# Kernel optimization log

Measured on AMD Instinct MI355X. Metric: run time of the kernel, lower is better.

Reference implementation:

```python
import jax, jax.numpy as jnp
import numpy as np

NUM_HEADS, HEAD_DIM = 4, 64
BLOCK_SIZE, S = 32, 4
LENGTHS = np.array([2048, 1024, 1536, 512, 2048, 1280, 1792, 768])
MAX_LEN = int(LENGTHS.max())            # 2048
NUM_BLOCKS = MAX_LEN // BLOCK_SIZE      # 64
B = len(LENGTHS)
T = int(LENGTHS.sum())                  # 11008
HIDDEN = NUM_HEADS * HEAD_DIM           # 256
SCALE = HEAD_DIM ** -0.5
INV_SCALE = 1.0 / SCALE
EPS = 1e-6


def setup_inputs() -> dict:
    key = jax.random.key(0)
    ks = jax.random.split(key, 6)
    offsets = np.concatenate([[0], np.cumsum(LENGTHS)]).astype(np.int64)
    batch_ids = np.repeat(np.arange(B), LENGTHS).astype(np.int64)
    pos_ids = np.concatenate([np.arange(l) for l in LENGTHS]).astype(np.int64)
    shp = (T, NUM_HEADS, HEAD_DIM)
    return {
        "q": jax.random.normal(ks[0], shp, jnp.float32),
        "k": jax.random.normal(ks[1], shp, jnp.float32),
        "v": jax.random.normal(ks[2], shp, jnp.float32),
        "u": jax.random.normal(ks[3], shp, jnp.float32),
        "Wg_cmp": jax.random.normal(ks[4], (NUM_HEADS, HEAD_DIM), jnp.float32) * 0.1,
        "Wg_slc": jax.random.normal(ks[5], (NUM_HEADS, HEAD_DIM), jnp.float32) * 0.1,
        "x_offsets": jnp.asarray(offsets),
        "batch_ids": jnp.asarray(batch_ids),
        "pos_ids": jnp.asarray(pos_ids),
    }


def _silu(x):
    return x * jax.nn.sigmoid(x)


def _layer_norm(x):
    # non-affine LayerNorm over last dim, eps=1e-6
    mu = jnp.mean(x, -1, keepdims=True)
    var = jnp.mean(jnp.square(x - mu), -1, keepdims=True)
    return (x - mu) / jnp.sqrt(var + EPS)


def _forward(q, k, v, u, Wg_cmp, Wg_slc, x_offsets, batch_ids, pos_ids):
    # jagged -> padded dense [B, MAX_LEN, H, D]
    pad = lambda x: jnp.zeros((B, MAX_LEN, NUM_HEADS, HEAD_DIM), x.dtype).at[batch_ids, pos_ids].set(x)
    pq, pk, pv = pad(q), pad(k), pad(v)

    # gate model: per-head sigmoid linear gates from padded_q; g_slc is unused
    # by the original forward (the slc kernel never consumes it)
    g_cmp = jax.nn.sigmoid(jnp.einsum('bnhd,hd->bnh', pq, Wg_cmp))
    _g_slc = jax.nn.sigmoid(jnp.einsum('bnhd,hd->bnh', pq, Wg_slc))
    g_cmp_jag = g_cmp[batch_ids, pos_ids]  # [T, H]

    # block-compressed K/V: mean over zero-padded blocks of size BLOCK_SIZE
    k_cmp = pk.reshape(B, NUM_BLOCKS, BLOCK_SIZE, NUM_HEADS, HEAD_DIM).mean(2)
    v_cmp = pv.reshape(B, NUM_BLOCKS, BLOCK_SIZE, NUM_HEADS, HEAD_DIM).mean(2)

    # SiLU-activated block-causal compressed attention
    raw = jnp.einsum('bnhd,bmhd->bnhm', pq, k_cmp) * SCALE  # [B, n, H, m]
    q_blk = jnp.arange(MAX_LEN) // BLOCK_SIZE
    k_blk = jnp.arange(NUM_BLOCKS)
    causal = q_blk[:, None] >= k_blk[None, :]   # [MAX_LEN, NUM_BLOCKS]
    local = q_blk[:, None] == k_blk[None, :]
    p_cmp = jnp.where(causal[None, :, None, :], _silu(raw) * INV_SCALE, 0.0)

    # top-S block selection; local block score forced to 1.0; odd slots
    # duplicated from even slots (as in source)
    sel = jnp.where(local[None, :, None, :], 1.0, p_cmp)
    topk = jax.lax.top_k(sel, S)[1]             # [B, MAX_LEN, H, S]
    topk = topk.at[..., 1::2].set(topk[..., 0::2])
    topk_jag = topk[batch_ids, pos_ids]         # [T, H, S]

    # compressed-branch output, gathered to jagged and gated by g_cmp
    o_cmp = jnp.einsum('bnhm,bmhd->bnhd', p_cmp, v_cmp)[batch_ids, pos_ids]
    o_cmp = o_cmp * g_cmp_jag[:, :, None]       # [T, H, D]

    # selected branch: per-row, per-head gather of S blocks of raw K/V
    seq_start = x_offsets[batch_ids]            # [T]
    head_ix = jnp.arange(NUM_HEADS)[None, :, None]
    o_slc = jnp.zeros_like(q)
    for s in range(S):  # fixed small S, duplicates intentionally double-count
        b_idx = topk_jag[:, :, s]               # [T, H]
        pos_in_seq = b_idx[:, :, None] * BLOCK_SIZE + jnp.arange(BLOCK_SIZE)  # [T,H,BS]
        valid = (b_idx[:, :, None] >= 0) & (pos_in_seq <= pos_ids[:, None, None])
        tgt = jnp.clip(seq_start[:, None, None] + pos_in_seq, 0, T - 1)
        k_g = k[tgt, head_ix]                   # [T, H, BS, D]
        score = jnp.einsum('thd,thbd->thb', q, k_g) * SCALE
        p = jnp.where(valid, _silu(score) * INV_SCALE, 0.0)
        v_g = v[tgt, head_ix]                   # [T, H, BS, D]
        o_slc = o_slc + jnp.einsum('thb,thbd->thd', p, v_g)

    # per-token LayerNorm over hidden, scaled by u, then branch sum
    o_cmp = _layer_norm(o_cmp.reshape(T, HIDDEN)).reshape(T, NUM_HEADS, HEAD_DIM) * u
    o_slc = _layer_norm(o_slc.reshape(T, HIDDEN)).reshape(T, NUM_HEADS, HEAD_DIM) * u
    return (o_cmp + o_slc).reshape(T, HIDDEN)


def reference(q, k, v, u, Wg_cmp, Wg_slc, x_offsets, batch_ids, pos_ids):
    return _forward(q, k, v, u, Wg_cmp, Wg_slc, x_offsets, batch_ids, pos_ids)
```

## Files before the change

### kernel.cpp

```cpp
#include <hip/hip_runtime.h>
#include <math.h>

#define NH 4
#define HD 64
#define HIDDEN 256
#define BS 32
#define NB 64
#define SCALE 0.125f
#define INV_SCALE 8.0f

__device__ __forceinline__ float fast_sigmoid(float x) {
    return 1.0f / (1.0f + __expf(-x));
}
__device__ __forceinline__ float readlane_f(float v, int lane) {
    return __int_as_float(__builtin_amdgcn_readlane(__float_as_int(v), lane));
}

__global__ __launch_bounds__(256) void kcmp_kernel(
    const float* __restrict__ k, const float* __restrict__ v,
    const int* __restrict__ x_offsets,
    double* __restrict__ k_cmp, float* __restrict__ v_cmp2) {
    int bb  = blockIdx.x;
    int b   = bb >> 6;
    int blk = bb & 63;
    int tid = threadIdx.x;
    int s0   = x_offsets[b];
    int len  = x_offsets[b + 1] - s0;
    int nblk = len >> 5;
    int h = tid >> 6, d = tid & 63;
    if (blockIdx.y == 0) {
        double acc = 0.0;
        if (blk < nblk) {
            const float* kp = k + (size_t)(s0 + blk * BS) * HIDDEN + tid;
            #pragma unroll
            for (int i = 0; i < BS; ++i) acc += (double)kp[i * HIDDEN];
            acc *= (1.0 / BS);
        }
        k_cmp[((size_t)(b * NH + h) * 64 + blk) * 64 + d] = acc;
    } else {
        float acc = 0.f;
        if (blk < nblk) {
            const float* vp = v + (size_t)(s0 + blk * BS) * HIDDEN + tid;
            #pragma unroll
            for (int i = 0; i < BS; ++i) acc += vp[i * HIDDEN];
            acc *= (1.0f / BS);
        }
        v_cmp2[((size_t)(b * NH + h) * 32 + (blk >> 1)) * 128 + d * 2 + (blk & 1)] = acc;
    }
}

__global__ __launch_bounds__(256, 3) void cmp_kernel(
    const float* __restrict__ q,
    const int* __restrict__ batch_ids, const int* __restrict__ pos_ids,
    const double* __restrict__ k_cmp, const float* __restrict__ v_cmp2,
    float* __restrict__ oc_buf, int2* __restrict__ idxbuf, int T) {
    int t0   = blockIdx.x * 64;
    int h    = blockIdx.y;
    int tid  = threadIdx.x;
    int wv   = __builtin_amdgcn_readfirstlane(tid >> 6);
    int lane = tid & 63;
    int b    = batch_ids[t0];
    int pos0 = pos_ids[t0];

    __shared__ __align__(16) char smem[49920];
    float* qs = (float*)smem;
    float* ps = qs + 64 * 65;
    float* vs = ps + 64 * 66;
    unsigned long long* trip = (unsigned long long*)qs;

    const float* qg = q + (size_t)t0 * HIDDEN + h * HD;
    #pragma unroll
    for (int i = 0; i < 16; ++i) {
        int idx = tid + 256 * i;
        int tok = idx >> 6, dd = idx & 63;
        qs[dd * 65 + tok] = qg[(size_t)tok * HIDDEN + dd];
    }
    const float* vg = v_cmp2 + (size_t)(b * NH + h) * 4096;
    #pragma unroll
    for (int i = 0; i < 16; ++i) vs[tid + 256 * i] = vg[tid + 256 * i];
    __syncthreads();

    int qblk_max = (pos0 + 63) >> 5;
    int m_need   = qblk_max + 2;
    if (m_need > 63) m_need = 63;

    unsigned long long a0 = 0ull, a1 = 0ull, a2 = 0ull;
    if (16 * wv <= m_need) {
        double qd[64];
        #pragma unroll
        for (int dd = 0; dd < 64; ++dd) qd[dd] = (double)qs[dd * 65 + lane];
        int myqblk = (pos0 + lane) >> 5;

        const double* kcb = k_cmp + ((size_t)(b * NH + h) * 64 + wv * 16) * 64;
        #pragma unroll
        for (int mi = 0; mi < 16; ++mi) {
            int m = wv * 16 + mi;
            const double* kr = kcb + mi * 64;
            double accA = 0.0, accB = 0.0;
            #pragma unroll
            for (int dd = 0; dd < 32; ++dd) {
                accA += qd[2 * dd]     * kr[2 * dd];
                accB += qd[2 * dd + 1] * kr[2 * dd + 1];
            }
            double r = (accA + accB) * 0.125;
            double p64 = 0.0;
            if (m <= myqblk) p64 = r / (1.0 + exp(-r)) * 8.0;
            double selv = (m == myqblk) ? 1.0 : p64;
            ps[lane * 66 + m] = (float)p64;
            long long sb = __double_as_longlong(selv);
            unsigned long long kk = (unsigned long long)sb;
            kk = (sb < 0) ? ~kk : (kk | 0x8000000000000000ull);
            kk = (kk & ~63ull) | (unsigned long long)(63 - m);
            if (kk > a0)      { a2 = a1; a1 = a0; a0 = kk; }
            else if (kk > a1) { a2 = a1; a1 = kk; }
            else if (kk > a2) { a2 = kk; }
        }
    }
    __syncthreads();
    trip[(wv * 64 + lane) * 3 + 0] = a0;
    trip[(wv * 64 + lane) * 3 + 1] = a1;
    trip[(wv * 64 + lane) * 3 + 2] = a2;
    __syncthreads();

    if (wv == 0) {
        unsigned long long kk2[4][3];
        #pragma unroll
        for (int w = 0; w < 4; ++w)
            #pragma unroll
            for (int j = 0; j < 3; ++j)
                kk2[w][j] = trip[(w * 64 + lane) * 3 + j];
        int pp[4] = {0, 0, 0, 0};
        int outi[3];
        #pragma unroll
        for (int s = 0; s < 3; ++s) {
            unsigned long long best = 0ull; int bw = 0;
            #pragma unroll
            for (int w = 0; w < 4; ++w) {
                unsigned long long hd_ = (pp[w] == 0) ? kk2[w][0]
                                       : (pp[w] == 1) ? kk2[w][1] : kk2[w][2];
                if (hd_ > best) { best = hd_; bw = w; }
            }
            outi[s] = 63 - (int)(best & 63ull);
            #pragma unroll
            for (int w = 0; w < 4; ++w) if (w == bw) pp[w]++;
        }
        idxbuf[(size_t)(t0 + lane) * NH + h] = make_int2(outi[0], outi[2]);
    }

    float occ[16];
    #pragma unroll
    for (int tt = 0; tt < 16; ++tt) occ[tt] = 0.f;
    int mmax2 = qblk_max >> 1;
    const float2* vs2 = (const float2*)vs;
    for (int m2 = 0; m2 <= mmax2; ++m2) {
        float2 vv = vs2[m2 * 64 + lane];
        #pragma unroll
        for (int tt = 0; tt < 16; ++tt) {
            int tok = wv * 16 + tt;
            float2 pv = *(const float2*)(ps + tok * 66 + 2 * m2);
            occ[tt] += pv.x * vv.x + pv.y * vv.y;
        }
    }
    #pragma unroll
    for (int tt = 0; tt < 16; ++tt)
        oc_buf[(size_t)(t0 + wv * 16 + tt) * HIDDEN + h * HD + lane] = occ[tt];
}

__global__ __launch_bounds__(64) void build_kernel(
    const int* __restrict__ pos_ids, const int2* __restrict__ idxbuf,
    int* __restrict__ cnt_arr, int2* __restrict__ entries,
    float* __restrict__ os_out, int T) {
    int wg   = blockIdx.x;
    int qb   = wg >> 2;
    int h    = wg & 3;
    int t0   = qb * 32;
    int lane = threadIdx.x;

    int pos0 = pos_ids[t0];
    int qblk = pos0 >> 5;

    float* ob = os_out + (size_t)t0 * HIDDEN + h * HD + lane;
    #pragma unroll
    for (int tk = 0; tk < 32; ++tk) ob[(size_t)tk * HIDDEN] = 0.f;

    int myi0 = -1, myi2 = -1;
    unsigned long long U = 0ull;
    if (lane < 32) {
        int2 ix = idxbuf[(size_t)(t0 + lane) * NH + h];
        myi0 = ix.x;
        myi2 = (ix.y <= qblk) ? ix.y : -1;
        U = (1ull << myi0);
        if (myi2 >= 0) U |= (1ull << myi2);
    }
    #pragma unroll
    for (int off = 1; off < 64; off <<= 1) U |= __shfl_xor(U, off, 64);

    int slot = 0;
    while (U) {
        int m = (int)__builtin_ctzll(U); U &= U - 1;
        unsigned long long wm = __ballot(lane < 32 && (myi0 == m || myi2 == m));
        if (lane == 0) entries[(size_t)wg * 64 + slot] = make_int2(m, (int)wm);
        slot++;
    }
    if (lane == 0) cnt_arr[wg] = slot;
}

__global__ __launch_bounds__(64, 4) void slc2_kernel(
    const float* __restrict__ q, const float* __restrict__ k,
    const float* __restrict__ v,
    const int* __restrict__ x_offsets, const int* __restrict__ batch_ids,
    const int* __restrict__ pos_ids,
    const int* __restrict__ cnt_arr, const int2* __restrict__ entries,
    float* __restrict__ os_out, int T) {
    int i  = blockIdx.x;
    int wgidx = (i & 7) * (gridDim.x >> 3) + (i >> 3);
    int slot = wgidx & 63;
    int wg   = wgidx >> 6;
    if (slot >= cnt_arr[wg]) return;

    int2 e = entries[(size_t)wg * 64 + slot];
    int m = e.x;
    unsigned int want = (unsigned int)e.y;
    int qb = wg >> 2, h = wg & 3;
    int t0 = qb * 32;
    int lane = threadIdx.x;
    int r = lane & 15, cc = lane >> 4;

    int pos0 = pos_ids[t0];
    int s0   = x_offsets[batch_ids[t0]];

    __shared__ float vs_w[32 * 64];

    const float* kb_p = k + (size_t)(s0 + m * BS) * HIDDEN + h * HD;
    float4 kb0[4], kb1[4];
    #pragma unroll
    for (int j = 0; j < 4; ++j) {
        kb0[j] = *(const float4*)(kb_p + (size_t)r * HIDDEN + (cc + 4 * j) * 4);
        kb1[j] = *(const float4*)(kb_p + (size_t)(16 + r) * HIDDEN + (cc + 4 * j) * 4);
    }
    {
        const float* vb_p = v + (size_t)(s0 + m * BS) * HIDDEN + h * HD + lane;
        #pragma unroll
        for (int g = 0; g < 4; ++g) {
            const float* p0_ = vb_p + (size_t)(g * 8) * HIDDEN;
            float x0 = p0_[0 * HIDDEN], x1 = p0_[1 * HIDDEN];
            float x2 = p0_[2 * HIDDEN], x3 = p0_[3 * HIDDEN];
            float x4 = p0_[4 * HIDDEN], x5 = p0_[5 * HIDDEN];
            float x6 = p0_[6 * HIDDEN], x7 = p0_[7 * HIDDEN];
            float* d0 = vs_w + (g * 8) * 64 + lane;
            d0[0 * 64] = x0; d0[1 * 64] = x1; d0[2 * 64] = x2; d0[3 * 64] = x3;
            d0[4 * 64] = x4; d0[5 * 64] = x5; d0[6 * 64] = x6; d0[7 * 64] = x7;
        }
    }
    #pragma unroll
    for (int j = 0; j < 4; ++j) {
        asm volatile("" : "+v"(kb0[j].x), "+v"(kb0[j].y),
                          "+v"(kb0[j].z), "+v"(kb0[j].w));
        asm volatile("" : "+v"(kb1[j].x), "+v"(kb1[j].y),
                          "+v"(kb1[j].z), "+v"(kb1[j].w));
    }
    int row0 = m * BS + r;

    while (want) {
        int tk0 = (int)__builtin_ctz(want); want &= want - 1;
        int tk1 = -1;
        if (want) { tk1 = (int)__builtin_ctz(want); want &= want - 1; }

        const float4* qr0 = (const float4*)(q + (size_t)(t0 + tk0) * HIDDEN + h * HD);
        const float4* qr1 = (tk1 >= 0)
            ? (const float4*)(q + (size_t)(t0 + tk1) * HIDDEN + h * HD) : qr0;
        float4 qa[4], qb[4];
        #pragma unroll
        for (int j = 0; j < 4; ++j) { qa[j] = qr0[cc + 4 * j]; qb[j] = qr1[cc + 4 * j]; }

        float pa0, pa1, pb0 = 0.f, pb1 = 0.f;
        {
            int pos_tk = pos0 + tk0;
            float psA0 = 0.f, psB0 = 0.f, psA1 = 0.f, psB1 = 0.f;
            #pragma unroll
            for (int j = 0; j < 4; ++j) {
                if (j & 1) {
                    psB0 += qa[j].x * kb0[j].x + qa[j].y * kb0[j].y
                          + qa[j].z * kb0[j].z + qa[j].w * kb0[j].w;
                    psB1 += qa[j].x * kb1[j].x + qa[j].y * kb1[j].y
                          + qa[j].z * kb1[j].z + qa[j].w * kb1[j].w;
                } else {
                    psA0 += qa[j].x * kb0[j].x + qa[j].y * kb0[j].y
                          + qa[j].z * kb0[j].z + qa[j].w * kb0[j].w;
                    psA1 += qa[j].x * kb1[j].x + qa[j].y * kb1[j].y
                          + qa[j].z * kb1[j].z + qa[j].w * kb1[j].w;
                }
            }
            float psum0 = psA0 + psB0, psum1 = psA1 + psB1;
            psum0 += __shfl_xor(psum0, 16, 64); psum0 += __shfl_xor(psum0, 32, 64);
            psum1 += __shfl_xor(psum1, 16, 64); psum1 += __shfl_xor(psum1, 32, 64);
            float scv0 = psum0 * SCALE, scv1 = psum1 * SCALE;
            pa0 = (row0 <= pos_tk)      ? scv0 * fast_sigmoid(scv0) * 16.f : 0.f;
            pa1 = (row0 + 16 <= pos_tk) ? scv1 * fast_sigmoid(scv1) * 16.f : 0.f;
        }
        if (tk1 >= 0) {
            int pos_tk = pos0 + tk1;
            float psA0 = 0.f, psB0 = 0.f, psA1 = 0.f, psB1 = 0.f;
            #pragma unroll
            for (int j = 0; j < 4; ++j) {
                if (j & 1) {
                    psB0 += qb[j].x * kb0[j].x + qb[j].y * kb0[j].y
                          + qb[j].z * kb0[j].z + qb[j].w * kb0[j].w;
                    psB1 += qb[j].x * kb1[j].x + qb[j].y * kb1[j].y
                          + qb[j].z * kb1[j].z + qb[j].w * kb1[j].w;
                } else {
                    psA0 += qb[j].x * kb0[j].x + qb[j].y * kb0[j].y
                          + qb[j].z * kb0[j].z + qb[j].w * kb0[j].w;
                    psA1 += qb[j].x * kb1[j].x + qb[j].y * kb1[j].y
                          + qb[j].z * kb1[j].z + qb[j].w * kb1[j].w;
                }
            }
            float psum0 = psA0 + psB0, psum1 = psA1 + psB1;
            psum0 += __shfl_xor(psum0, 16, 64); psum0 += __shfl_xor(psum0, 32, 64);
            psum1 += __shfl_xor(psum1, 16, 64); psum1 += __shfl_xor(psum1, 32, 64);
            float scv0 = psum0 * SCALE, scv1 = psum1 * SCALE;
            pb0 = (row0 <= pos_tk)      ? scv0 * fast_sigmoid(scv0) * 16.f : 0.f;
            pb1 = (row0 + 16 <= pos_tk) ? scv1 * fast_sigmoid(scv1) * 16.f : 0.f;
        }

        float oA0 = 0.f, oA1 = 0.f, oB0 = 0.f, oB1 = 0.f;
        #pragma unroll
        for (int rr = 0; rr < 16; ++rr) {
            float v0 = vs_w[rr * 64 + lane];
            float v1 = vs_w[(16 + rr) * 64 + lane];
            oA0 += readlane_f(pa0, rr) * v0;  oA1 += readlane_f(pa1, rr) * v1;
            oB0 += readlane_f(pb0, rr) * v0;  oB1 += readlane_f(pb1, rr) * v1;
        }
        atomicAdd(&os_out[(size_t)(t0 + tk0) * HIDDEN + h * HD + lane], oA0 + oA1);
        if (tk1 >= 0)
            atomicAdd(&os_out[(size_t)(t0 + tk1) * HIDDEN + h * HD + lane], oB0 + oB1);
    }
}

__global__ __launch_bounds__(256) void ln_kernel(
    const float* __restrict__ q, const float* __restrict__ u,
    const float* __restrict__ Wg_cmp,
    const float* __restrict__ oc_buf, float* __restrict__ io, int T) {
    int tid = threadIdx.x;
    int grp = tid >> 5;
    int sub = tid & 31;
    int t   = blockIdx.x * 8 + grp;
    int D0  = sub * 8;

    const float4* qp = (const float4*)(q + (size_t)t * HIDDEN + D0);
    float4 qa = qp[0], qb = qp[1];
    const float4* wp = (const float4*)(Wg_cmp + D0);
    float4 wa = wp[0], wb = wp[1];
    float gp = qa.x * wa.x + qa.y * wa.y + qa.z * wa.z + qa.w * wa.w
             + qb.x * wb.x + qb.y * wb.y + qb.z * wb.z + qb.w * wb.w;
    gp += __shfl_xor(gp, 1, 64);
    gp += __shfl_xor(gp, 2, 64);
    gp += __shfl_xor(gp, 4, 64);
    float g = fast_sigmoid(gp);

    const float4* ocp = (const float4*)(oc_buf + (size_t)t * HIDDEN + D0);
    float4 oa = ocp[0], ob = ocp[1];
    oa.x *= g; oa.y *= g; oa.z *= g; oa.w *= g;
    ob.x *= g; ob.y *= g; ob.z *= g; ob.w *= g;
    float4* iop = (float4*)(io + (size_t)t * HIDDEN + D0);
    float4 sa = iop[0], sb = iop[1];

    float sc_ = oa.x + oa.y + oa.z + oa.w + ob.x + ob.y + ob.z + ob.w;
    float sc2 = oa.x * oa.x + oa.y * oa.y + oa.z * oa.z + oa.w * oa.w
              + ob.x * ob.x + ob.y * ob.y + ob.z * ob.z + ob.w * ob.w;
    float ss_ = sa.x + sa.y + sa.z + sa.w + sb.x + sb.y + sb.z + sb.w;
    float ss2 = sa.x * sa.x + sa.y * sa.y + sa.z * sa.z + sa.w * sa.w
              + sb.x * sb.x + sb.y * sb.y + sb.z * sb.z + sb.w * sb.w;
    #pragma unroll
    for (int off = 1; off < 32; off <<= 1) {
        sc_ += __shfl_xor(sc_, off, 64);
        sc2 += __shfl_xor(sc2, off, 64);
        ss_ += __shfl_xor(ss_, off, 64);
        ss2 += __shfl_xor(ss2, off, 64);
    }
    float muc  = sc_ * (1.0f / HIDDEN);
    float varc = sc2 * (1.0f / HIDDEN) - muc * muc;
    float mus  = ss_ * (1.0f / HIDDEN);
    float vars = ss2 * (1.0f / HIDDEN) - mus * mus;
    float rc = rsqrtf(varc + 1e-6f), rs = rsqrtf(vars + 1e-6f);

    const float4* up = (const float4*)(u + (size_t)t * HIDDEN + D0);
    float4 ua = up[0], ub = up[1];
    float4 o0, o1;
    o0.x = ((oa.x - muc) * rc + (sa.x - mus) * rs) * ua.x;
    o0.y = ((oa.y - muc) * rc + (sa.y - mus) * rs) * ua.y;
    o0.z = ((oa.z - muc) * rc + (sa.z - mus) * rs) * ua.z;
    o0.w = ((oa.w - muc) * rc + (sa.w - mus) * rs) * ua.w;
    o1.x = ((ob.x - muc) * rc + (sb.x - mus) * rs) * ub.x;
    o1.y = ((ob.y - muc) * rc + (sb.y - mus) * rs) * ub.y;
    o1.z = ((ob.z - muc) * rc + (sb.z - mus) * rs) * ub.z;
    o1.w = ((ob.w - muc) * rc + (sb.w - mus) * rs) * ub.w;
    iop[0] = o0; iop[1] = o1;
}

extern "C" void kernel_launch(void* const* d_in, const int* in_sizes, int n_in,
                              void* d_out, int out_size, void* d_ws, size_t ws_size,
                              hipStream_t stream) {
    const float* q      = (const float*)d_in[0];
    const float* k      = (const float*)d_in[1];
    const float* v      = (const float*)d_in[2];
    const float* u      = (const float*)d_in[3];
    const float* Wg_cmp = (const float*)d_in[4];
    const int* x_offsets = (const int*)d_in[6];
    const int* batch_ids = (const int*)d_in[7];
    const int* pos_ids   = (const int*)d_in[8];

    int T = in_sizes[0] / HIDDEN;
    int B = in_sizes[6] - 1;

    double* k_cmp  = (double*)d_ws;
    float*  v_cmp2 = (float*)(k_cmp + (size_t)B * NH * 4096);
    float*  oc_buf = v_cmp2 + (size_t)B * NH * 4096;
    int2*   idxbuf = (int2*)(oc_buf + (size_t)T * HIDDEN);
    int2*   entries = idxbuf + (size_t)T * NH;
    int*    cnt_arr = (int*)(entries + (size_t)(T / 32) * NH * 64);

    int nwg = (T / 32) * NH;

    kcmp_kernel<<<dim3(B * NB, 2), 256, 0, stream>>>(k, v, x_offsets, k_cmp, v_cmp2);
    cmp_kernel<<<dim3(T / 64, NH), 256, 0, stream>>>(
        q, batch_ids, pos_ids, k_cmp, v_cmp2, oc_buf, idxbuf, T);
    build_kernel<<<dim3(nwg), 64, 0, stream>>>(
        pos_ids, idxbuf, cnt_arr, entries, (float*)d_out, T);
    slc2_kernel<<<dim3(nwg * 64), 64, 0, stream>>>(
        q, k, v, x_offsets, batch_ids, pos_ids, cnt_arr, entries,
        (float*)d_out, T);
    ln_kernel<<<dim3(T / 8), 256, 0, stream>>>(
        q, u, Wg_cmp, oc_buf, (float*)d_out, T);
}
```

Baseline: 208.3 us.

## Compact selection entries and use persistent work-stealing grid for selection kernel

```diff
diff --git a/kernel.cpp b/kernel.cpp
--- a/kernel.cpp
+++ b/kernel.cpp
@@ -19,11 +19,13 @@
 __global__ __launch_bounds__(256) void kcmp_kernel(
     const float* __restrict__ k, const float* __restrict__ v,
     const int* __restrict__ x_offsets,
-    double* __restrict__ k_cmp, float* __restrict__ v_cmp2) {
+    double* __restrict__ k_cmp, float* __restrict__ v_cmp2,
+    int* __restrict__ counters) {
     int bb  = blockIdx.x;
     int b   = bb >> 6;
     int blk = bb & 63;
     int tid = threadIdx.x;
+    if (bb == 0 && blockIdx.y == 0 && tid < 2) counters[tid] = 0;
     int s0   = x_offsets[b];
     int len  = x_offsets[b + 1] - s0;
     int nblk = len >> 5;
@@ -168,7 +170,7 @@
 
 __global__ __launch_bounds__(64) void build_kernel(
     const int* __restrict__ pos_ids, const int2* __restrict__ idxbuf,
-    int* __restrict__ cnt_arr, int2* __restrict__ entries,
+    int* __restrict__ counters, int2* __restrict__ entries,
     float* __restrict__ os_out, int T) {
     int wg   = blockIdx.x;
     int qb   = wg >> 2;
@@ -195,145 +197,154 @@
     #pragma unroll
     for (int off = 1; off < 64; off <<= 1) U |= __shfl_xor(U, off, 64);
 
+    int nsel = __popcll(U);
+    int base = 0;
+    if (lane == 0) base = atomicAdd(&counters[0], nsel);
+    base = __shfl(base, 0, 64);
+
     int slot = 0;
     while (U) {
         int m = (int)__builtin_ctzll(U); U &= U - 1;
         unsigned long long wm = __ballot(lane < 32 && (myi0 == m || myi2 == m));
-        if (lane == 0) entries[(size_t)wg * 64 + slot] = make_int2(m, (int)wm);
+        if (lane == 0)
+            entries[(size_t)base + slot] = make_int2((wg << 6) | m, (int)wm);
         slot++;
     }
-    if (lane == 0) cnt_arr[wg] = slot;
-}
-
-__global__ __launch_bounds__(64, 4) void slc2_kernel(
+}
+
+__global__ __launch_bounds__(64, 4) void slc3_kernel(
     const float* __restrict__ q, const float* __restrict__ k,
     const float* __restrict__ v,
     const int* __restrict__ x_offsets, const int* __restrict__ batch_ids,
     const int* __restrict__ pos_ids,
-    const int* __restrict__ cnt_arr, const int2* __restrict__ entries,
+    int* __restrict__ counters, const int2* __restrict__ entries,
     float* __restrict__ os_out, int T) {
-    int i  = blockIdx.x;
-    int wgidx = (i & 7) * (gridDim.x >> 3) + (i >> 3);
-    int slot = wgidx & 63;
-    int wg   = wgidx >> 6;
-    if (slot >= cnt_arr[wg]) return;
-
-    int2 e = entries[(size_t)wg * 64 + slot];
-    int m = e.x;
-    unsigned int want = (unsigned int)e.y;
-    int qb = wg >> 2, h = wg & 3;
-    int t0 = qb * 32;
     int lane = threadIdx.x;
     int r = lane & 15, cc = lane >> 4;
-
-    int pos0 = pos_ids[t0];
-    int s0   = x_offsets[batch_ids[t0]];
-
     __shared__ float vs_w[32 * 64];
 
-    const float* kb_p = k + (size_t)(s0 + m * BS) * HIDDEN + h * HD;
-    float4 kb0[4], kb1[4];
-    #pragma unroll
-    for (int j = 0; j < 4; ++j) {
-        kb0[j] = *(const float4*)(kb_p + (size_t)r * HIDDEN + (cc + 4 * j) * 4);
-        kb1[j] = *(const float4*)(kb_p + (size_t)(16 + r) * HIDDEN + (cc + 4 * j) * 4);
-    }
-    {
-        const float* vb_p = v + (size_t)(s0 + m * BS) * HIDDEN + h * HD + lane;
-        #pragma unroll
-        for (int g = 0; g < 4; ++g) {
-            const float* p0_ = vb_p + (size_t)(g * 8) * HIDDEN;
-            float x0 = p0_[0 * HIDDEN], x1 = p0_[1 * HIDDEN];
-            float x2 = p0_[2 * HIDDEN], x3 = p0_[3 * HIDDEN];
-            float x4 = p0_[4 * HIDDEN], x5 = p0_[5 * HIDDEN];
-            float x6 = p0_[6 * HIDDEN], x7 = p0_[7 * HIDDEN];
-            float* d0 = vs_w + (g * 8) * 64 + lane;
-            d0[0 * 64] = x0; d0[1 * 64] = x1; d0[2 * 64] = x2; d0[3 * 64] = x3;
-            d0[4 * 64] = x4; d0[5 * 64] = x5; d0[6 * 64] = x6; d0[7 * 64] = x7;
-        }
-    }
-    #pragma unroll
-    for (int j = 0; j < 4; ++j) {
-        asm volatile("" : "+v"(kb0[j].x), "+v"(kb0[j].y),
-                          "+v"(kb0[j].z), "+v"(kb0[j].w));
-        asm volatile("" : "+v"(kb1[j].x), "+v"(kb1[j].y),
-                          "+v"(kb1[j].z), "+v"(kb1[j].w));
-    }
-    int row0 = m * BS + r;
-
-    while (want) {
-        int tk0 = (int)__builtin_ctz(want); want &= want - 1;
-        int tk1 = -1;
-        if (want) { tk1 = (int)__builtin_ctz(want); want &= want - 1; }
-
-        const float4* qr0 = (const float4*)(q + (size_t)(t0 + tk0) * HIDDEN + h * HD);
-        const float4* qr1 = (tk1 >= 0)
-            ? (const float4*)(q + (size_t)(t0 + tk1) * HIDDEN + h * HD) : qr0;
-        float4 qa[4], qb[4];
-        #pragma unroll
-        for (int j = 0; j < 4; ++j) { qa[j] = qr0[cc + 4 * j]; qb[j] = qr1[cc + 4 * j]; }
-
-        float pa0, pa1, pb0 = 0.f, pb1 = 0.f;
+    int total = counters[0];
+
+    for (;;) {
+        int t_ = 0;
+        if (lane == 0) t_ = atomicAdd(&counters[1], 1);
+        t_ = __shfl(t_, 0, 64);
+        if (t_ >= total) break;
+
+        int2 e = entries[t_];
+        int wg = e.x >> 6;
+        int m  = e.x & 63;
+        unsigned int want = (unsigned int)e.y;
+        int qb = wg >> 2, h = wg & 3;
+        int t0 = qb * 32;
+
+        int pos0 = pos_ids[t0];
+        int s0   = x_offsets[batch_ids[t0]];
+
+        const float* kb_p = k + (size_t)(s0 + m * BS) * HIDDEN + h * HD;
+        float4 kb0[4], kb1[4];
+        #pragma unroll
+        for (int j = 0; j < 4; ++j) {
+            kb0[j] = *(const float4*)(kb_p + (size_t)r * HIDDEN + (cc + 4 * j) * 4);
+            kb1[j] = *(const float4*)(kb_p + (size_t)(16 + r) * HIDDEN + (cc + 4 * j) * 4);
+        }
         {
-            int pos_tk = pos0 + tk0;
-            float psA0 = 0.f, psB0 = 0.f, psA1 = 0.f, psB1 = 0.f;
-            #pragma unroll
-            for (int j = 0; j < 4; ++j) {
-                if (j & 1) {
-                    psB0 += qa[j].x * kb0[j].x + qa[j].y * kb0[j].y
-                          + qa[j].z * kb0[j].z + qa[j].w * kb0[j].w;
-                    psB1 += qa[j].x * kb1[j].x + qa[j].y * kb1[j].y
-                          + qa[j].z * kb1[j].z + qa[j].w * kb1[j].w;
-                } else {
-                    psA0 += qa[j].x * kb0[j].x + qa[j].y * kb0[j].y
-                          + qa[j].z * kb0[j].z + qa[j].w * kb0[j].w;
-                    psA1 += qa[j].x * kb1[j].x + qa[j].y * kb1[j].y
-                          + qa[j].z * kb1[j].z + qa[j].w * kb1[j].w;
+            const float* vb_p = v + (size_t)(s0 + m * BS) * HIDDEN + h * HD + lane;
+            #pragma unroll
+            for (int g = 0; g < 4; ++g) {
+                const float* p0_ = vb_p + (size_t)(g * 8) * HIDDEN;
+                float x0 = p0_[0 * HIDDEN], x1 = p0_[1 * HIDDEN];
+                float x2 = p0_[2 * HIDDEN], x3 = p0_[3 * HIDDEN];
+                float x4 = p0_[4 * HIDDEN], x5 = p0_[5 * HIDDEN];
+                float x6 = p0_[6 * HIDDEN], x7 = p0_[7 * HIDDEN];
+                float* d0 = vs_w + (g * 8) * 64 + lane;
+                d0[0 * 64] = x0; d0[1 * 64] = x1; d0[2 * 64] = x2; d0[3 * 64] = x3;
+                d0[4 * 64] = x4; d0[5 * 64] = x5; d0[6 * 64] = x6; d0[7 * 64] = x7;
+            }
+        }
+        #pragma unroll
+        for (int j = 0; j < 4; ++j) {
+            asm volatile("" : "+v"(kb0[j].x), "+v"(kb0[j].y),
+                              "+v"(kb0[j].z), "+v"(kb0[j].w));
+            asm volatile("" : "+v"(kb1[j].x), "+v"(kb1[j].y),
+                              "+v"(kb1[j].z), "+v"(kb1[j].w));
+        }
+        int row0 = m * BS + r;
+
+        while (want) {
+            int tk0 = (int)__builtin_ctz(want); want &= want - 1;
+            int tk1 = -1;
+            if (want) { tk1 = (int)__builtin_ctz(want); want &= want - 1; }
+
+            const float4* qr0 = (const float4*)(q + (size_t)(t0 + tk0) * HIDDEN + h * HD);
+            const float4* qr1 = (tk1 >= 0)
+                ? (const float4*)(q + (size_t)(t0 + tk1) * HIDDEN + h * HD) : qr0;
+            float4 qv0[4], qv1[4];
+            #pragma unroll
+            for (int j = 0; j < 4; ++j) { qv0[j] = qr0[cc + 4 * j]; qv1[j] = qr1[cc + 4 * j]; }
+
+            float pa0, pa1, pb0 = 0.f, pb1 = 0.f;
+            {
+                int pos_tk = pos0 + tk0;
+                float psA0 = 0.f, psB0 = 0.f, psA1 = 0.f, psB1 = 0.f;
+                #pragma unroll
+                for (int j = 0; j < 4; ++j) {
+                    if (j & 1) {
+                        psB0 += qv0[j].x * kb0[j].x + qv0[j].y * kb0[j].y
+                              + qv0[j].z * kb0[j].z + qv0[j].w * kb0[j].w;
+                        psB1 += qv0[j].x * kb1[j].x + qv0[j].y * kb1[j].y
+                              + qv0[j].z * kb1[j].z + qv0[j].w * kb1[j].w;
+                    } else {
+                        psA0 += qv0[j].x * kb0[j].x + qv0[j].y * kb0[j].y
+                              + qv0[j].z * kb0[j].z + qv0[j].w * kb0[j].w;
+                        psA1 += qv0[j].x * kb1[j].x + qv0[j].y * kb1[j].y
+                              + qv0[j].z * kb1[j].z + qv0[j].w * kb1[j].w;
+                    }
                 }
-            }
-            float psum0 = psA0 + psB0, psum1 = psA1 + psB1;
-            psum0 += __shfl_xor(psum0, 16, 64); psum0 += __shfl_xor(psum0, 32, 64);
-            psum1 += __shfl_xor(psum1, 16, 64); psum1 += __shfl_xor(psum1, 32, 64);
-            float scv0 = psum0 * SCALE, scv1 = psum1 * SCALE;
-            pa0 = (row0 <= pos_tk)      ? scv0 * fast_sigmoid(scv0) * 16.f : 0.f;
-            pa1 = (row0 + 16 <= pos_tk) ? scv1 * fast_sigmoid(scv1) * 16.f : 0.f;
-        }
-        if (tk1 >= 0) {
-            int pos_tk = pos0 + tk1;
-            float psA0 = 0.f, psB0 = 0.f, psA1 = 0.f, psB1 = 0.f;
-            #pragma unroll
-            for (int j = 0; j < 4; ++j) {
-                if (j & 1) {
-                    psB0 += qb[j].x * kb0[j].x + qb[j].y * kb0[j].y
-                          + qb[j].z * kb0[j].z + qb[j].w * kb0[j].w;
-                    psB1 += qb[j].x * kb1[j].x + qb[j].y * kb1[j].y
-                          + qb[j].z * kb1[j].z + qb[j].w * kb1[j].w;
-                } else {
-                    psA0 += qb[j].x * kb0[j].x + qb[j].y * kb0[j].y
-                          + qb[j].z * kb0[j].z + qb[j].w * kb0[j].w;
-                    psA1 += qb[j].x * kb1[j].x + qb[j].y * kb1[j].y
-                          + qb[j].z * kb1[j].z + qb[j].w * kb1[j].w;
+                float psum0 = psA0 + psB0, psum1 = psA1 + psB1;
+                psum0 += __shfl_xor(psum0, 16, 64); psum0 += __shfl_xor(psum0, 32, 64);
+                psum1 += __shfl_xor(psum1, 16, 64); psum1 += __shfl_xor(psum1, 32, 64);
+                float scv0 = psum0 * SCALE, scv1 = psum1 * SCALE;
+                pa0 = (row0 <= pos_tk)      ? scv0 * fast_sigmoid(scv0) * 16.f : 0.f;
+                pa1 = (row0 + 16 <= pos_tk) ? scv1 * fast_sigmoid(scv1) * 16.f : 0.f;
+            }
+            if (tk1 >= 0) {
+                int pos_tk = pos0 + tk1;
+                float psA0 = 0.f, psB0 = 0.f, psA1 = 0.f, psB1 = 0.f;
+                #pragma unroll
+                for (int j = 0; j < 4; ++j) {
+                    if (j & 1) {
+                        psB0 += qv1[j].x * kb0[j].x + qv1[j].y * kb0[j].y
+                              + qv1[j].z * kb0[j].z + qv1[j].w * kb0[j].w;
+                        psB1 += qv1[j].x * kb1[j].x + qv1[j].y * kb1[j].y
+                              + qv1[j].z * kb1[j].z + qv1[j].w * kb1[j].w;
+                    } else {
+                        psA0 += qv1[j].x * kb0[j].x + qv1[j].y * kb0[j].y
+                              + qv1[j].z * kb0[j].z + qv1[j].w * kb0[j].w;
+                        psA1 += qv1[j].x * kb1[j].x + qv1[j].y * kb1[j].y
+                              + qv1[j].z * kb1[j].z + qv1[j].w * kb1[j].w;
+                    }
                 }
-            }
-            float psum0 = psA0 + psB0, psum1 = psA1 + psB1;
-            psum0 += __shfl_xor(psum0, 16, 64); psum0 += __shfl_xor(psum0, 32, 64);
-            psum1 += __shfl_xor(psum1, 16, 64); psum1 += __shfl_xor(psum1, 32, 64);
-            float scv0 = psum0 * SCALE, scv1 = psum1 * SCALE;
-            pb0 = (row0 <= pos_tk)      ? scv0 * fast_sigmoid(scv0) * 16.f : 0.f;
-            pb1 = (row0 + 16 <= pos_tk) ? scv1 * fast_sigmoid(scv1) * 16.f : 0.f;
-        }
-
-        float oA0 = 0.f, oA1 = 0.f, oB0 = 0.f, oB1 = 0.f;
-        #pragma unroll
-        for (int rr = 0; rr < 16; ++rr) {
-            float v0 = vs_w[rr * 64 + lane];
-            float v1 = vs_w[(16 + rr) * 64 + lane];
-            oA0 += readlane_f(pa0, rr) * v0;  oA1 += readlane_f(pa1, rr) * v1;
-            oB0 += readlane_f(pb0, rr) * v0;  oB1 += readlane_f(pb1, rr) * v1;
-        }
-        atomicAdd(&os_out[(size_t)(t0 + tk0) * HIDDEN + h * HD + lane], oA0 + oA1);
-        if (tk1 >= 0)
-            atomicAdd(&os_out[(size_t)(t0 + tk1) * HIDDEN + h * HD + lane], oB0 + oB1);
+                float psum0 = psA0 + psB0, psum1 = psA1 + psB1;
+                psum0 += __shfl_xor(psum0, 16, 64); psum0 += __shfl_xor(psum0, 32, 64);
+                psum1 += __shfl_xor(psum1, 16, 64); psum1 += __shfl_xor(psum1, 32, 64);
+                float scv0 = psum0 * SCALE, scv1 = psum1 * SCALE;
+                pb0 = (row0 <= pos_tk)      ? scv0 * fast_sigmoid(scv0) * 16.f : 0.f;
+                pb1 = (row0 + 16 <= pos_tk) ? scv1 * fast_sigmoid(scv1) * 16.f : 0.f;
+            }
+
+            float oA0 = 0.f, oA1 = 0.f, oB0 = 0.f, oB1 = 0.f;
+            #pragma unroll
+            for (int rr = 0; rr < 16; ++rr) {
+                float v0 = vs_w[rr * 64 + lane];
+                float v1 = vs_w[(16 + rr) * 64 + lane];
+                oA0 += readlane_f(pa0, rr) * v0;  oA1 += readlane_f(pa1, rr) * v1;
+                oB0 += readlane_f(pb0, rr) * v0;  oB1 += readlane_f(pb1, rr) * v1;
+            }
+            atomicAdd(&os_out[(size_t)(t0 + tk0) * HIDDEN + h * HD + lane], oA0 + oA1);
+            if (tk1 >= 0)
+                atomicAdd(&os_out[(size_t)(t0 + tk1) * HIDDEN + h * HD + lane], oB0 + oB1);
+        }
     }
 }
 
@@ -418,17 +429,18 @@
     float*  oc_buf = v_cmp2 + (size_t)B * NH * 4096;
     int2*   idxbuf = (int2*)(oc_buf + (size_t)T * HIDDEN);
     int2*   entries = idxbuf + (size_t)T * NH;
-    int*    cnt_arr = (int*)(entries + (size_t)(T / 32) * NH * 64);
+    int*    counters = (int*)(entries + (size_t)(T / 32) * NH * 64);
 
     int nwg = (T / 32) * NH;
 
-    kcmp_kernel<<<dim3(B * NB, 2), 256, 0, stream>>>(k, v, x_offsets, k_cmp, v_cmp2);
+    kcmp_kernel<<<dim3(B * NB, 2), 256, 0, stream>>>(
+        k, v, x_offsets, k_cmp, v_cmp2, counters);
     cmp_kernel<<<dim3(T / 64, NH), 256, 0, stream>>>(
         q, batch_ids, pos_ids, k_cmp, v_cmp2, oc_buf, idxbuf, T);
     build_kernel<<<dim3(nwg), 64, 0, stream>>>(
-        pos_ids, idxbuf, cnt_arr, entries, (float*)d_out, T);
-    slc2_kernel<<<dim3(nwg * 64), 64, 0, stream>>>(
-        q, k, v, x_offsets, batch_ids, pos_ids, cnt_arr, entries,
+        pos_ids, idxbuf, counters, entries, (float*)d_out, T);
+    slc3_kernel<<<dim3(4096), 64, 0, stream>>>(
+        q, k, v, x_offsets, batch_ids, pos_ids, counters, entries,
         (float*)d_out, T);
     ln_kernel<<<dim3(T / 8), 256, 0, stream>>>(
         q, u, Wg_cmp, oc_buf, (float*)d_out, T);
```

Result: slower. 545.3 us (+161.8%).
